# Kernel tuning notes

Hardware: AMD Instinct MI355X
Metric: run time of the kernel (lower is better)

The kernel has to match this reference:

```python
import jax, jax.numpy as jnp
import numpy as np

NEG_INF = -9e15  # matches -9000000000000000.0 in the torch source


def setup_inputs() -> dict:
    key = jax.random.key(0)
    k1, k2, k3, k4 = jax.random.split(key, 4)
    B, H, N, D = 4, 8, 2048, 64
    queries = jax.random.normal(k1, (B, H, N, D), dtype=jnp.float32)
    keys = jax.random.normal(k2, (B, H, N, D), dtype=jnp.float32)
    values = jax.random.normal(k3, (B, H, N, D), dtype=jnp.float32)
    adj = jax.random.randint(k4, (N, N), 0, 2, dtype=jnp.int32)
    return {"queries": queries, "keys": keys, "values": values, "adj": adj}


def reference(queries, keys, values, adj):
    B, H, N, D = queries.shape
    # e = Q K^T / 8  (hard-coded divisor == sqrt(64))
    e = jnp.einsum("bhnd,bhmd->bhnm", queries, keys) / 8.0
    # graph-adjacency mask (adj [N,N] broadcasts over batch and heads)
    att = jnp.where(adj > 0, e, NEG_INF)
    att = jax.nn.softmax(att, axis=-1)
    # dropout p=0.0 / eval mode -> identity
    h_prime = jnp.einsum("bhnm,bhmd->bhnd", att, values)  # [B,H,N,D]
    # original uses .view (flat reshape), NOT a permute
    return h_prime.reshape(N, B, H, D)
```

## Files before the change

### kernel.cpp

```cpp
#include <hip/hip_runtime.h>
#include <math.h>

typedef short short8 __attribute__((ext_vector_type(8)));
typedef float float4_t __attribute__((ext_vector_type(4)));
typedef float f32x16 __attribute__((ext_vector_type(16)));
typedef unsigned short ushort_t;

#define BH   32
#define N_   2048
#define D_   64
#define NCH  32
#define KV_ELEMS (BH * N_ * D_)
#define OFF_VF  (KV_ELEMS * 2)
#define OFF_MSK (KV_ELEMS * 4)
#define QSCALE 0.18033688f

__device__ __forceinline__ unsigned pack_bf16(float a, float b) {
  union { float f; unsigned u; } ua{a}, ub{b};
  return __builtin_amdgcn_perm(ub.u + 0x8000u, ua.u + 0x8000u, 0x07060302u);
}

__device__ __forceinline__ unsigned cvt_pk_bf16(float a, float b) {
  unsigned r;
  asm("v_cvt_pk_bf16_f32 %0, %1, %2" : "=v"(r) : "v"(a), "v"(b));
  return r;
}

__device__ __forceinline__ void gload_lds16(const ushort_t* g, ushort_t* l) {
  __builtin_amdgcn_global_load_lds(
      (const __attribute__((address_space(1))) unsigned int*)(g),
      (__attribute__((address_space(3))) unsigned int*)(l), 16, 0, 0);
}

__global__ __launch_bounds__(256) void prep_kernel(
    const float* __restrict__ K, const float* __restrict__ V,
    const int* __restrict__ adj, ushort_t* __restrict__ Kf,
    ushort_t* __restrict__ Vf, unsigned long long* __restrict__ msk) {
  __shared__ __align__(16) float Tc[64 * 68];
  const int blk = blockIdx.x, t = threadIdx.x;

  if (blk < 2048) {
    const bool isK = blk < 1024;
    const int b = isK ? blk : blk - 1024;
    const float* src = (isK ? K : V) + (b >> 5) * (N_ * D_) + (b & 31) * 64 * D_;
#pragma unroll
    for (int i = 0; i < 4; ++i) {
      int idx = i * 256 + t;
      int row = idx >> 4, c4 = (idx & 15) * 4;
      *(float4_t*)&Tc[row * 68 + c4] = *(const float4_t*)(src + row * D_ + c4);
    }
    __syncthreads();
    ushort_t* dst = (isK ? Kf : Vf) + b * 4096;
#pragma unroll
    for (int e = 0; e < 2; ++e) {
      int u = t * 2 + e;
      int g = u >> 6, lane = u & 63;
      int hi = lane >> 5, l32 = lane & 31;
      float v[8];
      if (isK) {
        int nt = g >> 2, ks = g & 3;
        const float* rp = &Tc[(nt * 32 + l32) * 68 + ks * 16 + hi * 8];
        float4_t a = *(const float4_t*)(rp);
        float4_t bq = *(const float4_t*)(rp + 4);
#pragma unroll
        for (int j = 0; j < 4; ++j) { v[j] = a[j]; v[4 + j] = bq[j]; }
      } else {
        int nt = g >> 2, dt = (g >> 1) & 1, ksp = g & 1;
#pragma unroll
        for (int j = 0; j < 8; ++j) {
          int key = (ksp * 2 + (j >> 2)) * 8 + hi * 4 + (j & 3);
          v[j] = Tc[(nt * 32 + key) * 68 + dt * 32 + l32];
        }
      }
      union { short8 s; unsigned u4[4]; } h;
      h.u4[0] = pack_bf16(v[0], v[1]); h.u4[1] = pack_bf16(v[2], v[3]);
      h.u4[2] = pack_bf16(v[4], v[5]); h.u4[3] = pack_bf16(v[6], v[7]);
      *(short8*)(dst + u * 8) = h.s;
    }
  } else {
    const int row = (blk - 2048) * 4 + (t >> 6);
    const int lane = t & 63;
    unsigned long long keep = 0;
#pragma unroll 8
    for (int i = 0; i < 32; ++i) {
      int a = adj[row * N_ + i * 64 + lane];
      unsigned long long b = __ballot(a > 0);
      if (lane == i) keep = b;
    }
    if (lane < 32) msk[(size_t)lane * 2048 + row] = keep;
  }
}

__global__ __launch_bounds__(512, 4) void attn_main(
    const float* __restrict__ Q, const ushort_t* __restrict__ Kf,
    const ushort_t* __restrict__ Vf, const unsigned long long* __restrict__ msk,
    float* __restrict__ O) {
  __shared__ __align__(16) ushort_t kv[2][8192];
  __shared__ float xbuf[4][32][64];

  const int t    = threadIdx.x;
  const int w    = t >> 6;
  const int lane = t & 63;
  const int l32  = lane & 31;
  const int hi   = lane >> 5;
  const int pair = w >> 1;
  const int nt   = w & 1;
  const int bh   = blockIdx.x & (BH - 1);
  const int qt   = blockIdx.x >> 5;
  const int base = bh * (N_ * D_);
  const int trow0 = qt * 128 + pair * 32;

  const ushort_t* Kfb = Kf + (bh * 32) * 4096;
  const ushort_t* Vfb = Vf + (bh * 32) * 4096;
  const unsigned long long* mrow = msk + (trow0 + l32);

  short8 qf[4];
#pragma unroll
  for (int ks = 0; ks < 4; ++ks) {
    const float* qp = Q + base + (trow0 + l32) * D_ + ks * 16 + hi * 8;
    float4_t f0 = *(const float4_t*)(qp);
    float4_t f1 = *(const float4_t*)(qp + 4);
    union { short8 s; unsigned u[4]; } h;
    h.u[0] = pack_bf16(f0[0] * QSCALE, f0[1] * QSCALE);
    h.u[1] = pack_bf16(f0[2] * QSCALE, f0[3] * QSCALE);
    h.u[2] = pack_bf16(f1[0] * QSCALE, f1[1] * QSCALE);
    h.u[3] = pack_bf16(f1[2] * QSCALE, f1[3] * QSCALE);
    qf[ks] = h.s;
  }

  short8 ones;
#pragma unroll
  for (int j = 0; j < 8; ++j) ones[j] = (short)0x3F80;

  f32x16 oacc0, oacc1;
  f32x16 osacc;
#pragma unroll
  for (int i = 0; i < 16; ++i) { oacc0[i] = 0.f; oacc1[i] = 0.f; osacc[i] = 0.f; }

  const int fo = lane * 8;

#define STAGE(nb, c)                                                          \
  do {                                                                        \
    const ushort_t* _s = (w < 4 ? Kfb + (c)*4096 + w * 1024                   \
                                : Vfb + (c)*4096 + (w - 4) * 1024) + lane * 8;\
    ushort_t* _d = &kv[nb][w * 1024];                                         \
    gload_lds16(_s, _d);                                                      \
    gload_lds16(_s + 512, _d + 512);                                          \
  } while (0)

  STAGE(0, 0);

#pragma unroll 2
  for (int c = 0; c < NCH; ++c) {
    const int cur = c & 1;
    __syncthreads();

    unsigned long long mw = mrow[(size_t)c * 2048];

    if (c + 1 < NCH) STAGE(cur ^ 1, c + 1);

    const ushort_t* kb = &kv[cur][0];
    const ushort_t* vb = &kv[cur][4096];

    f32x16 sacc;
#pragma unroll
    for (int i = 0; i < 16; ++i) sacc[i] = 0.f;
#pragma unroll
    for (int ks = 0; ks < 4; ++ks) {
      short8 kfr = *(const short8*)(kb + (nt * 4 + ks) * 512 + fo);
      sacc = __builtin_amdgcn_mfma_f32_32x32x16_bf16(kfr, qf[ks], sacc, 0, 0, 0);
    }

    unsigned half = (unsigned)(nt ? (mw >> 32) : mw);
    half >>= (hi << 2);
    float p[16];
#pragma unroll
    for (int reg = 0; reg < 16; ++reg) {
      const int pos = (reg & 3) + 8 * (reg >> 2);
      int sm = ((int)(half << (31 - pos))) >> 31;
      union { float f; unsigned u; } e;
      e.f = __builtin_amdgcn_exp2f(sacc[reg]);
      e.u &= (unsigned)sm;
      p[reg] = e.f;
    }

    union { short8 s; unsigned u[4]; } pa0, pa1;
#pragma unroll
    for (int jj = 0; jj < 4; ++jj) {
      int r = (jj >> 1) * 4 + (jj & 1) * 2;
      pa0.u[jj] = cvt_pk_bf16(p[r], p[r + 1]);
      pa1.u[jj] = cvt_pk_bf16(p[8 + r], p[8 + r + 1]);
    }

    {
      short8 v00 = *(const short8*)(vb + (nt * 4 + 0) * 512 + fo);
      short8 v01 = *(const short8*)(vb + (nt * 4 + 1) * 512 + fo);
      short8 v10 = *(const short8*)(vb + (nt * 4 + 2) * 512 + fo);
      short8 v11 = *(const short8*)(vb + (nt * 4 + 3) * 512 + fo);
      oacc0 = __builtin_amdgcn_mfma_f32_32x32x16_bf16(pa0.s, v00, oacc0, 0, 0, 0);
      oacc0 = __builtin_amdgcn_mfma_f32_32x32x16_bf16(pa1.s, v01, oacc0, 0, 0, 0);
      oacc1 = __builtin_amdgcn_mfma_f32_32x32x16_bf16(pa0.s, v10, oacc1, 0, 0, 0);
      oacc1 = __builtin_amdgcn_mfma_f32_32x32x16_bf16(pa1.s, v11, oacc1, 0, 0, 0);
      osacc = __builtin_amdgcn_mfma_f32_32x32x16_bf16(pa0.s, ones, osacc, 0, 0, 0);
      osacc = __builtin_amdgcn_mfma_f32_32x32x16_bf16(pa1.s, ones, osacc, 0, 0, 0);
    }
  }

  __syncthreads();
  if (nt) {
#pragma unroll
    for (int reg = 0; reg < 16; ++reg) {
      xbuf[pair][reg][lane]      = oacc0[reg];
      xbuf[pair][16 + reg][lane] = osacc[reg];
    }
  }
  __syncthreads();
  float invv[16];
  if (!nt) {
#pragma unroll
    for (int reg = 0; reg < 16; ++reg) {
      invv[reg] = 1.f / (osacc[reg] + xbuf[pair][16 + reg][lane]);
      oacc0[reg] = (oacc0[reg] + xbuf[pair][reg][lane]) * invv[reg];
    }
  }
  __syncthreads();
  if (nt) {
#pragma unroll
    for (int reg = 0; reg < 16; ++reg) xbuf[pair][reg][lane] = oacc1[reg];
  }
  __syncthreads();
  if (!nt) {
#pragma unroll
    for (int reg = 0; reg < 16; ++reg) {
      int qo = (reg & 3) + 8 * (reg >> 2) + 4 * hi;
      O[base + (trow0 + qo) * D_ + l32]      = oacc0[reg];
      O[base + (trow0 + qo) * D_ + 32 + l32] =
          (oacc1[reg] + xbuf[pair][reg][lane]) * invv[reg];
    }
  }
}

extern "C" void kernel_launch(void* const* d_in, const int* in_sizes, int n_in,
                              void* d_out, int out_size, void* d_ws, size_t ws_size,
                              hipStream_t stream) {
  const float* Q  = (const float*)d_in[0];
  const float* K  = (const float*)d_in[1];
  const float* V  = (const float*)d_in[2];
  const int* adj  = (const int*)d_in[3];
  float* O        = (float*)d_out;
  ushort_t* Kf    = (ushort_t*)d_ws;
  ushort_t* Vf    = (ushort_t*)((char*)d_ws + OFF_VF);
  unsigned long long* msk = (unsigned long long*)((char*)d_ws + OFF_MSK);

  prep_kernel<<<2560, 256, 0, stream>>>(K, V, adj, Kf, Vf, msk);
  attn_main<<<512, 512, 0, stream>>>(Q, Kf, Vf, msk, O);
}
```

Baseline: 152.3 us.

## Software-pipeline QK^T one chunk ahead with a 4-slot LDS ring

```diff
diff --git a/kernel.cpp b/kernel.cpp
--- a/kernel.cpp
+++ b/kernel.cpp
@@ -95,8 +95,9 @@
     const float* __restrict__ Q, const ushort_t* __restrict__ Kf,
     const ushort_t* __restrict__ Vf, const unsigned long long* __restrict__ msk,
     float* __restrict__ O) {
-  __shared__ __align__(16) ushort_t kv[2][8192];
-  __shared__ float xbuf[4][32][64];
+  __shared__ __align__(16) char smem[65536];
+  ushort_t (*kv)[8192] = (ushort_t (*)[8192])smem;
+  float (*xbuf)[32][64] = (float (*)[32][64])smem;
 
   const int t    = threadIdx.x;
   const int w    = t >> 6;
@@ -148,62 +149,61 @@
     gload_lds16(_s + 512, _d + 512);                                          \
   } while (0)
 
+#define SCOMP(SACC, cc)                                                       \
+  do {                                                                        \
+    const ushort_t* _kb = &kv[(cc) & 3][0];                                   \
+    _Pragma("unroll") for (int _i = 0; _i < 16; ++_i) SACC[_i] = 0.f;         \
+    _Pragma("unroll") for (int _ks = 0; _ks < 4; ++_ks) {                     \
+      short8 _kfr = *(const short8*)(_kb + (nt * 4 + _ks) * 512 + fo);        \
+      SACC = __builtin_amdgcn_mfma_f32_32x32x16_bf16(_kfr, qf[_ks], SACC, 0, 0, 0); \
+    }                                                                         \
+  } while (0)
+
+#define BODY(c, SCUR, SNEXT)                                                  \
+  {                                                                           \
+    __syncthreads();   \
+    unsigned long long mw = mrow[(size_t)(c) * 2048];                         \
+    if ((c) + 2 < NCH) STAGE(((c) + 2) & 3, (c) + 2);                         \
+    if ((c) + 1 < NCH) SCOMP(SNEXT, (c) + 1);                                 \
+    unsigned half = (unsigned)(nt ? (mw >> 32) : mw);                         \
+    half >>= (hi << 2);                                                       \
+    float p[16];                                                              \
+    _Pragma("unroll") for (int reg = 0; reg < 16; ++reg) {                    \
+      const int pos = (reg & 3) + 8 * (reg >> 2);                             \
+      int sm = ((int)(half << (31 - pos))) >> 31;                             \
+      union { float f; unsigned u; } e;                                       \
+      e.f = __builtin_amdgcn_exp2f(SCUR[reg]);                                \
+      e.u &= (unsigned)sm;                                                    \
+      p[reg] = e.f;                                                           \
+    }                                                                         \
+    union { short8 s; unsigned u[4]; } pa0, pa1;                              \
+    _Pragma("unroll") for (int jj = 0; jj < 4; ++jj) {                        \
+      int r = (jj >> 1) * 4 + (jj & 1) * 2;                                   \
+      pa0.u[jj] = cvt_pk_bf16(p[r], p[r + 1]);                                \
+      pa1.u[jj] = cvt_pk_bf16(p[8 + r], p[8 + r + 1]);                        \
+    }                                                                         \
+    const ushort_t* vb = &kv[(c) & 3][4096];                                  \
+    short8 v00 = *(const short8*)(vb + (nt * 4 + 0) * 512 + fo);              \
+    short8 v01 = *(const short8*)(vb + (nt * 4 + 1) * 512 + fo);              \
+    short8 v10 = *(const short8*)(vb + (nt * 4 + 2) * 512 + fo);              \
+    short8 v11 = *(const short8*)(vb + (nt * 4 + 3) * 512 + fo);              \
+    oacc0 = __builtin_amdgcn_mfma_f32_32x32x16_bf16(pa0.s, v00, oacc0, 0, 0, 0); \
+    oacc0 = __builtin_amdgcn_mfma_f32_32x32x16_bf16(pa1.s, v01, oacc0, 0, 0, 0); \
+    oacc1 = __builtin_amdgcn_mfma_f32_32x32x16_bf16(pa0.s, v10, oacc1, 0, 0, 0); \
+    oacc1 = __builtin_amdgcn_mfma_f32_32x32x16_bf16(pa1.s, v11, oacc1, 0, 0, 0); \
+    osacc = __builtin_amdgcn_mfma_f32_32x32x16_bf16(pa0.s, ones, osacc, 0, 0, 0); \
+    osacc = __builtin_amdgcn_mfma_f32_32x32x16_bf16(pa1.s, ones, osacc, 0, 0, 0); \
+  }
+
   STAGE(0, 0);
-
-#pragma unroll 2
-  for (int c = 0; c < NCH; ++c) {
-    const int cur = c & 1;
-    __syncthreads();
-
-    unsigned long long mw = mrow[(size_t)c * 2048];
-
-    if (c + 1 < NCH) STAGE(cur ^ 1, c + 1);
-
-    const ushort_t* kb = &kv[cur][0];
-    const ushort_t* vb = &kv[cur][4096];
-
-    f32x16 sacc;
-#pragma unroll
-    for (int i = 0; i < 16; ++i) sacc[i] = 0.f;
-#pragma unroll
-    for (int ks = 0; ks < 4; ++ks) {
-      short8 kfr = *(const short8*)(kb + (nt * 4 + ks) * 512 + fo);
-      sacc = __builtin_amdgcn_mfma_f32_32x32x16_bf16(kfr, qf[ks], sacc, 0, 0, 0);
-    }
-
-    unsigned half = (unsigned)(nt ? (mw >> 32) : mw);
-    half >>= (hi << 2);
-    float p[16];
-#pragma unroll
-    for (int reg = 0; reg < 16; ++reg) {
-      const int pos = (reg & 3) + 8 * (reg >> 2);
-      int sm = ((int)(half << (31 - pos))) >> 31;
-      union { float f; unsigned u; } e;
-      e.f = __builtin_amdgcn_exp2f(sacc[reg]);
-      e.u &= (unsigned)sm;
-      p[reg] = e.f;
-    }
-
-    union { short8 s; unsigned u[4]; } pa0, pa1;
-#pragma unroll
-    for (int jj = 0; jj < 4; ++jj) {
-      int r = (jj >> 1) * 4 + (jj & 1) * 2;
-      pa0.u[jj] = cvt_pk_bf16(p[r], p[r + 1]);
-      pa1.u[jj] = cvt_pk_bf16(p[8 + r], p[8 + r + 1]);
-    }
-
-    {
-      short8 v00 = *(const short8*)(vb + (nt * 4 + 0) * 512 + fo);
-      short8 v01 = *(const short8*)(vb + (nt * 4 + 1) * 512 + fo);
-      short8 v10 = *(const short8*)(vb + (nt * 4 + 2) * 512 + fo);
-      short8 v11 = *(const short8*)(vb + (nt * 4 + 3) * 512 + fo);
-      oacc0 = __builtin_amdgcn_mfma_f32_32x32x16_bf16(pa0.s, v00, oacc0, 0, 0, 0);
-      oacc0 = __builtin_amdgcn_mfma_f32_32x32x16_bf16(pa1.s, v01, oacc0, 0, 0, 0);
-      oacc1 = __builtin_amdgcn_mfma_f32_32x32x16_bf16(pa0.s, v10, oacc1, 0, 0, 0);
-      oacc1 = __builtin_amdgcn_mfma_f32_32x32x16_bf16(pa1.s, v11, oacc1, 0, 0, 0);
-      osacc = __builtin_amdgcn_mfma_f32_32x32x16_bf16(pa0.s, ones, osacc, 0, 0, 0);
-      osacc = __builtin_amdgcn_mfma_f32_32x32x16_bf16(pa1.s, ones, osacc, 0, 0, 0);
-    }
+  STAGE(1, 1);
+  __syncthreads();
+  f32x16 saccA, saccB;
+  SCOMP(saccA, 0);
+
+  for (int c = 0; c < NCH; c += 2) {
+    BODY(c,     saccA, saccB);
+    BODY(c + 1, saccB, saccA);
   }
 
   __syncthreads();
```

After: 155.4 us. 1.02x slower.

## Load K/V fragments directly from global instead of LDS double-buffer

Applied to the files above, without the earlier changes.

```diff
diff --git a/kernel.cpp b/kernel.cpp
--- a/kernel.cpp
+++ b/kernel.cpp
@@ -24,12 +24,6 @@
   unsigned r;
   asm("v_cvt_pk_bf16_f32 %0, %1, %2" : "=v"(r) : "v"(a), "v"(b));
   return r;
-}
-
-__device__ __forceinline__ void gload_lds16(const ushort_t* g, ushort_t* l) {
-  __builtin_amdgcn_global_load_lds(
-      (const __attribute__((address_space(1))) unsigned int*)(g),
-      (__attribute__((address_space(3))) unsigned int*)(l), 16, 0, 0);
 }
 
 __global__ __launch_bounds__(256) void prep_kernel(
@@ -95,7 +89,6 @@
     const float* __restrict__ Q, const ushort_t* __restrict__ Kf,
     const ushort_t* __restrict__ Vf, const unsigned long long* __restrict__ msk,
     float* __restrict__ O) {
-  __shared__ __align__(16) ushort_t kv[2][8192];
   __shared__ float xbuf[4][32][64];
 
   const int t    = threadIdx.x;
@@ -139,37 +132,24 @@
 
   const int fo = lane * 8;
 
-#define STAGE(nb, c)                                                          \
-  do {                                                                        \
-    const ushort_t* _s = (w < 4 ? Kfb + (c)*4096 + w * 1024                   \
-                                : Vfb + (c)*4096 + (w - 4) * 1024) + lane * 8;\
-    ushort_t* _d = &kv[nb][w * 1024];                                         \
-    gload_lds16(_s, _d);                                                      \
-    gload_lds16(_s + 512, _d + 512);                                          \
-  } while (0)
-
-  STAGE(0, 0);
-
 #pragma unroll 2
   for (int c = 0; c < NCH; ++c) {
-    const int cur = c & 1;
-    __syncthreads();
-
+    const ushort_t* kg = Kfb + c * 4096 + nt * 2048 + fo;
+    const ushort_t* vg = Vfb + c * 4096 + nt * 2048 + fo;
+
+    short8 kfr[4], vfr[4];
+#pragma unroll
+    for (int ks = 0; ks < 4; ++ks) kfr[ks] = *(const short8*)(kg + ks * 512);
+#pragma unroll
+    for (int j = 0; j < 4; ++j)   vfr[j] = *(const short8*)(vg + j * 512);
     unsigned long long mw = mrow[(size_t)c * 2048];
 
-    if (c + 1 < NCH) STAGE(cur ^ 1, c + 1);
-
-    const ushort_t* kb = &kv[cur][0];
-    const ushort_t* vb = &kv[cur][4096];
-
     f32x16 sacc;
 #pragma unroll
     for (int i = 0; i < 16; ++i) sacc[i] = 0.f;
 #pragma unroll
-    for (int ks = 0; ks < 4; ++ks) {
-      short8 kfr = *(const short8*)(kb + (nt * 4 + ks) * 512 + fo);
-      sacc = __builtin_amdgcn_mfma_f32_32x32x16_bf16(kfr, qf[ks], sacc, 0, 0, 0);
-    }
+    for (int ks = 0; ks < 4; ++ks)
+      sacc = __builtin_amdgcn_mfma_f32_32x32x16_bf16(kfr[ks], qf[ks], sacc, 0, 0, 0);
 
     unsigned half = (unsigned)(nt ? (mw >> 32) : mw);
     half >>= (hi << 2);
@@ -192,18 +172,12 @@
       pa1.u[jj] = cvt_pk_bf16(p[8 + r], p[8 + r + 1]);
     }
 
-    {
-      short8 v00 = *(const short8*)(vb + (nt * 4 + 0) * 512 + fo);
-      short8 v01 = *(const short8*)(vb + (nt * 4 + 1) * 512 + fo);
-      short8 v10 = *(const short8*)(vb + (nt * 4 + 2) * 512 + fo);
-      short8 v11 = *(const short8*)(vb + (nt * 4 + 3) * 512 + fo);
-      oacc0 = __builtin_amdgcn_mfma_f32_32x32x16_bf16(pa0.s, v00, oacc0, 0, 0, 0);
-      oacc0 = __builtin_amdgcn_mfma_f32_32x32x16_bf16(pa1.s, v01, oacc0, 0, 0, 0);
-      oacc1 = __builtin_amdgcn_mfma_f32_32x32x16_bf16(pa0.s, v10, oacc1, 0, 0, 0);
-      oacc1 = __builtin_amdgcn_mfma_f32_32x32x16_bf16(pa1.s, v11, oacc1, 0, 0, 0);
-      osacc = __builtin_amdgcn_mfma_f32_32x32x16_bf16(pa0.s, ones, osacc, 0, 0, 0);
-      osacc = __builtin_amdgcn_mfma_f32_32x32x16_bf16(pa1.s, ones, osacc, 0, 0, 0);
-    }
+    oacc0 = __builtin_amdgcn_mfma_f32_32x32x16_bf16(pa0.s, vfr[0], oacc0, 0, 0, 0);
+    oacc0 = __builtin_amdgcn_mfma_f32_32x32x16_bf16(pa1.s, vfr[1], oacc0, 0, 0, 0);
+    oacc1 = __builtin_amdgcn_mfma_f32_32x32x16_bf16(pa0.s, vfr[2], oacc1, 0, 0, 0);
+    oacc1 = __builtin_amdgcn_mfma_f32_32x32x16_bf16(pa1.s, vfr[3], oacc1, 0, 0, 0);
+    osacc = __builtin_amdgcn_mfma_f32_32x32x16_bf16(pa0.s, ones, osacc, 0, 0, 0);
+    osacc = __builtin_amdgcn_mfma_f32_32x32x16_bf16(pa1.s, ones, osacc, 0, 0, 0);
   }
 
   __syncthreads();
```

New measurement: 177.3 us. 16.4% more time.
